# Optimization experiments

Measured on AMD Instinct MI355X. Metric: run time of the kernel, lower is better.

## Reference

```python
import jax, jax.numpy as jnp
import numpy as np

N = 200000      # total nodes
H = 256         # hidden dim
G = 512         # number of graphs (segments)


def setup_inputs() -> dict:
    key = jax.random.key(0)
    ks = jax.random.split(key, 6)
    x = jax.random.normal(ks[0], (N, H), dtype=jnp.float32)
    batch = jnp.sort(jax.random.randint(ks[1], (N,), 0, G, dtype=jnp.int64))
    # attn_gate: Linear(H, H//2) -> Tanh -> Linear(H//2, 1)
    W1 = jax.random.normal(ks[2], (H, H // 2), dtype=jnp.float32) * (1.0 / np.sqrt(H))
    b1 = jnp.zeros((H // 2,), dtype=jnp.float32)
    W2 = jax.random.normal(ks[3], (H // 2, 1), dtype=jnp.float32) * (1.0 / np.sqrt(H // 2))
    b2 = jnp.zeros((1,), dtype=jnp.float32)
    # context_proj: Linear(H, H)
    Wp = jax.random.normal(ks[4], (H, H), dtype=jnp.float32) * (1.0 / np.sqrt(H))
    bp = jnp.zeros((H,), dtype=jnp.float32)
    return {"x": x, "batch": batch, "W1": W1, "b1": b1, "W2": W2, "b2": b2, "Wp": Wp, "bp": bp}


def reference(x, batch, W1, b1, W2, b2, Wp, bp):
    # gating MLP -> per-node scalar score [N, 1]
    s = jnp.tanh(x @ W1 + b1) @ W2 + b2
    # scatter_softmax over segments (numerically stable)
    seg_max = jax.ops.segment_max(s, batch, num_segments=G)        # [G, 1]
    e = jnp.exp(s - seg_max[batch])                                 # [N, 1]
    seg_sum = jax.ops.segment_sum(e, batch, num_segments=G)        # [G, 1]
    w = e / seg_sum[batch]                                          # [N, 1]
    # attention-weighted global add pool -> [G, H]
    graph_emb = jax.ops.segment_sum(x * w, batch, num_segments=G)
    # project and broadcast back to nodes -> [N, H]
    context = graph_emb @ Wp + bp
    return context[batch]
```

## Files before the change

kernel.cpp:

```cpp
#include <hip/hip_runtime.h>
#include <hip/hip_bf16.h>

#define HH 256
#define HJ 128
#define GG 512

typedef __attribute__((ext_vector_type(8))) short short8;
typedef __attribute__((ext_vector_type(4))) float f32x4;

static __device__ __forceinline__ unsigned f2bfu(float f) {
  unsigned u = __builtin_bit_cast(unsigned, f);
  return (u + 0x7FFFu + ((u >> 16) & 1u)) >> 16;
}

static __device__ __forceinline__ uint2 pack4(const float4 f) {
  return make_uint2(f2bfu(f.x) | (f2bfu(f.y) << 16),
                    f2bfu(f.z) | (f2bfu(f.w) << 16));
}

__global__ __launch_bounds__(64) void w1frag_kernel(
    const float* __restrict__ W1, short8* __restrict__ w1a) {
  const int l = threadIdx.x;
  const int kt = blockIdx.x >> 3;
  const int jt = blockIdx.x & 7;
  const int j = jt * 16 + (l & 15);
  const int kb = kt * 32 + (l >> 4) * 8;
  short8 v;
#pragma unroll
  for (int i = 0; i < 8; ++i) v[i] = (short)f2bfu(W1[(size_t)(kb + i) * HJ + j]);
  w1a[blockIdx.x * 64 + l] = v;
}

__global__ __launch_bounds__(256) void segstart_kernel(
    const int* __restrict__ batch, int* __restrict__ segstart, int N, int G) {
  const int n = blockIdx.x * 256 + threadIdx.x;
  if (n >= N) return;
  const int b = batch[n];
  const int p = (n == 0) ? -1 : batch[n - 1];
  for (int g = p + 1; g <= b; ++g) segstart[g] = n;
  if (n == N - 1) {
    for (int g = b + 1; g <= G; ++g) segstart[g] = N;
  }
}

__global__ __launch_bounds__(512) void fused_kernel(
    const float* __restrict__ x, const short8* __restrict__ w1a,
    const float* __restrict__ b1, const float* __restrict__ W2,
    const int* __restrict__ segstart, const float* __restrict__ Wp,
    const float* __restrict__ bp, float4* __restrict__ out4, int N) {
  __shared__ char xb[3 * 32768];
  __shared__ float spart[2][8][64];
  __shared__ float elds[64];
  __shared__ float esums;

  const int tid = threadIdx.x;
  const int l = tid & 63;
  const int w = tid >> 6;
  const int g = blockIdx.x;

  const int n0 = segstart[g];
  const int n1 = segstart[g + 1];
  const int cnt = n1 - n0;
  if (cnt <= 0) return;

  const int ntiles = (cnt + 63) >> 6;
  const float4* x4 = (const float4*)x;

  const int jt0 = w & 3;
  short8 afrag[2][8];
  float4 bb[2], ww[2];
  if (w < 4) {
#pragma unroll
    for (int jj = 0; jj < 2; ++jj) {
      const int jt = jt0 + jj * 4;
#pragma unroll
      for (int kt = 0; kt < 8; ++kt) afrag[jj][kt] = w1a[(kt * 8 + jt) * 64 + l];
      const int j0 = 16 * jt + (l >> 4) * 4;
      bb[jj] = *reinterpret_cast<const float4*>(b1 + j0);
      ww[jj] = *reinterpret_cast<const float4*>(W2 + j0);
    }
  }

  {
    float4 rr[8];
#pragma unroll
    for (int k = 0; k < 8; ++k) {
      const int node = min(n0 + w * 8 + k, N - 1);
      rr[k] = x4[(size_t)node * 64 + l];
    }
#pragma unroll
    for (int k = 0; k < 8; ++k) {
      const int r = w * 8 + k;
      const int swz = (r & 7) << 4;
      *reinterpret_cast<uint2*>(xb + r * 512 + ((l * 8) ^ swz)) = pack4(rr[k]);
    }
  }
  __syncthreads();

  const int c2 = tid & 127;
  const int qh = (tid >> 7) & 1;
  float2 pacc = make_float2(0.f, 0.f);
  float es_acc = 0.f;

  for (int i = 0; i < ntiles; ++i) {
    if (w < 4) {
      const char* xbi = xb + (i % 3) * 32768;
      float* sp = &spart[i & 1][0][0];
#pragma unroll
      for (int nt = 0; nt < 4; ++nt) {
        const int node = nt * 16 + (l & 15);
        const int nb = node * 512;
        const int swz = (node & 7) << 4;
        short8 bfrag[8];
#pragma unroll
        for (int kt = 0; kt < 8; ++kt) {
          bfrag[kt] = *reinterpret_cast<const short8*>(
              xbi + nb + ((kt * 64 + ((l >> 4) << 4)) ^ swz));
        }
#pragma unroll
        for (int jj = 0; jj < 2; ++jj) {
          f32x4 acc = (f32x4)(0.f);
#pragma unroll
          for (int kt = 0; kt < 8; ++kt) {
            acc = __builtin_amdgcn_mfma_f32_16x16x32_bf16(afrag[jj][kt],
                                                          bfrag[kt], acc, 0, 0, 0);
          }
          float t0 = __expf(2.f * (acc[0] + bb[jj].x));
          float t1 = __expf(2.f * (acc[1] + bb[jj].y));
          float t2 = __expf(2.f * (acc[2] + bb[jj].z));
          float t3 = __expf(2.f * (acc[3] + bb[jj].w));
          float ps = (1.f - 2.f / (t0 + 1.f)) * ww[jj].x +
                     (1.f - 2.f / (t1 + 1.f)) * ww[jj].y +
                     (1.f - 2.f / (t2 + 1.f)) * ww[jj].z +
                     (1.f - 2.f / (t3 + 1.f)) * ww[jj].w;
          ps += __shfl_xor(ps, 16, 64);
          ps += __shfl_xor(ps, 32, 64);
          if (l < 16) sp[(jt0 + jj * 4) * 64 + node] = ps;
        }
      }
    } else {
      if (i >= 1) {
        const float* sp = &spart[(i - 1) & 1][0][0];
        float s = 0.f;
#pragma unroll
        for (int jt = 0; jt < 8; ++jt) s += sp[jt * 64 + l];
        const int node = n0 + (i - 1) * 64 + l;
        const float e = (node < n1) ? __expf(s) : 0.f;
        elds[l] = e;
        if (w == 4) es_acc += e;
        const char* xbs = xb + ((i - 1) % 3) * 32768;
#pragma unroll 8
        for (int m = 0; m < 32; ++m) {
          const int n = qh * 32 + m;
          const unsigned v = *reinterpret_cast<const unsigned*>(
              xbs + n * 512 + ((c2 * 4) ^ ((n & 7) << 4)));
          const float ee = elds[n];
          pacc.x = fmaf(__builtin_bit_cast(float, v << 16), ee, pacc.x);
          pacc.y = fmaf(__builtin_bit_cast(float, v & 0xFFFF0000u), ee, pacc.y);
        }
      }
      if (i + 1 < ntiles) {
        char* xbd = xb + ((i + 1) % 3) * 32768;
        const int rb = (w - 4) * 16;
        float4 rr[8];
#pragma unroll
        for (int b = 0; b < 2; ++b) {
#pragma unroll
          for (int k = 0; k < 8; ++k) {
            const int node = min(n0 + (i + 1) * 64 + rb + b * 8 + k, N - 1);
            rr[k] = x4[(size_t)node * 64 + l];
          }
#pragma unroll
          for (int k = 0; k < 8; ++k) {
            const int r = rb + b * 8 + k;
            const int swz = (r & 7) << 4;
            *reinterpret_cast<uint2*>(xbd + r * 512 + ((l * 8) ^ swz)) =
                pack4(rr[k]);
          }
        }
      }
    }
    __syncthreads();
  }

  if (w >= 4) {
    const float* sp = &spart[(ntiles - 1) & 1][0][0];
    float s = 0.f;
#pragma unroll
    for (int jt = 0; jt < 8; ++jt) s += sp[jt * 64 + l];
    const int node = n0 + (ntiles - 1) * 64 + l;
    const float e = (node < n1) ? __expf(s) : 0.f;
    elds[l] = e;
    if (w == 4) es_acc += e;
    const char* xbs = xb + ((ntiles - 1) % 3) * 32768;
#pragma unroll 8
    for (int m = 0; m < 32; ++m) {
      const int n = qh * 32 + m;
      const unsigned v = *reinterpret_cast<const unsigned*>(
          xbs + n * 512 + ((c2 * 4) ^ ((n & 7) << 4)));
      const float ee = elds[n];
      pacc.x = fmaf(__builtin_bit_cast(float, v << 16), ee, pacc.x);
      pacc.y = fmaf(__builtin_bit_cast(float, v & 0xFFFF0000u), ee, pacc.y);
    }
    if (w == 4) {
      float es = es_acc;
      es += __shfl_xor(es, 1, 64);
      es += __shfl_xor(es, 2, 64);
      es += __shfl_xor(es, 4, 64);
      es += __shfl_xor(es, 8, 64);
      es += __shfl_xor(es, 16, 64);
      es += __shfl_xor(es, 32, 64);
      if (l == 0) esums = es;
    }
  }
  __syncthreads();

  float* fbase = (float*)xb;
  if (w >= 4) {
    fbase[qh * 256 + c2 * 2] = pacc.x;
    fbase[qh * 256 + c2 * 2 + 1] = pacc.y;
  }
  __syncthreads();

  float* er = fbase + 512;
  if (tid < HH) {
    const float es = esums;
    const float inv = (es > 0.f) ? 1.f / es : 0.f;
    er[tid] = (fbase[tid] + fbase[256 + tid]) * inv;
  }
  __syncthreads();

  float* pr = fbase + 768;
  {
    const int c = tid & 255;
    const int h2 = tid >> 8;
    float p = 0.f;
    const float* wp = Wp + (size_t)h2 * 128 * HH + c;
#pragma unroll 4
    for (int k = 0; k < 128; ++k) {
      p = fmaf(er[h2 * 128 + k], wp[(size_t)k * HH], p);
    }
    pr[h2 * 256 + c] = p;
  }
  __syncthreads();
  float* ctxl = fbase + 1280;
  if (tid < HH) {
    ctxl[tid] = pr[tid] + pr[256 + tid] + bp[tid];
  }
  __syncthreads();

  {
    const int q = tid & 63;
    const float4 cv = reinterpret_cast<const float4*>(ctxl)[q];
    for (int n = n0 + w; n < n1; n += 8) {
      out4[(size_t)n * 64 + q] = cv;
    }
  }
}

extern "C" void kernel_launch(void* const* d_in, const int* in_sizes, int n_in,
                              void* d_out, int out_size, void* d_ws, size_t ws_size,
                              hipStream_t stream) {
  const float* x = (const float*)d_in[0];
  const int* batch = (const int*)d_in[1];
  const float* W1 = (const float*)d_in[2];
  const float* b1 = (const float*)d_in[3];
  const float* W2 = (const float*)d_in[4];
  const float* Wp = (const float*)d_in[6];
  const float* bp = (const float*)d_in[7];
  float* out = (float*)d_out;

  const int N = in_sizes[1];
  const int G = GG;

  char* wsp = (char*)d_ws;
  short8* w1a = (short8*)wsp;
  size_t off = 4096 * sizeof(short8);
  int* segstart = (int*)(wsp + off);

  w1frag_kernel<<<dim3(64), 64, 0, stream>>>(W1, w1a);
  {
    dim3 grid((N + 255) / 256);
    segstart_kernel<<<grid, 256, 0, stream>>>(batch, segstart, N, G);
  }
  fused_kernel<<<dim3(G), 512, 0, stream>>>(x, w1a, b1, W2, segstart, Wp, bp,
                                            (float4*)out, N);
}
```

Baseline: 116.8 us.

## Double block size to 1024 threads with eight MFMA and eight pooling/loader waves

Each block now launches 1024 threads. Eight waves compute the gating MLP, one 16-column j-tile each, and eight waves handle softmax pooling and the prefetch of the next x tile, so each wave does half its former work. Wave n-tile order is rotated to spread LDS access. The Wp projection is split four ways and the output broadcast uses 16 waves. This shortens each block's serial critical path, but it limits occupancy to one block per CU and adds more sync overhead and register pressure.

```diff
diff --git a/kernel.cpp b/kernel.cpp
--- a/kernel.cpp
+++ b/kernel.cpp
@@ -43,7 +43,7 @@
   }
 }
 
-__global__ __launch_bounds__(512) void fused_kernel(
+__global__ __launch_bounds__(1024, 1) void fused_kernel(
     const float* __restrict__ x, const short8* __restrict__ w1a,
     const float* __restrict__ b1, const float* __restrict__ W2,
     const int* __restrict__ segstart, const float* __restrict__ Wp,
@@ -66,49 +66,46 @@
   const int ntiles = (cnt + 63) >> 6;
   const float4* x4 = (const float4*)x;
 
-  const int jt0 = w & 3;
-  short8 afrag[2][8];
-  float4 bb[2], ww[2];
-  if (w < 4) {
-#pragma unroll
-    for (int jj = 0; jj < 2; ++jj) {
-      const int jt = jt0 + jj * 4;
-#pragma unroll
-      for (int kt = 0; kt < 8; ++kt) afrag[jj][kt] = w1a[(kt * 8 + jt) * 64 + l];
-      const int j0 = 16 * jt + (l >> 4) * 4;
-      bb[jj] = *reinterpret_cast<const float4*>(b1 + j0);
-      ww[jj] = *reinterpret_cast<const float4*>(W2 + j0);
-    }
-  }
-
-  {
-    float4 rr[8];
-#pragma unroll
-    for (int k = 0; k < 8; ++k) {
-      const int node = min(n0 + w * 8 + k, N - 1);
+  short8 afrag[8];
+  float4 bb, ww;
+  if (w < 8) {
+#pragma unroll
+    for (int kt = 0; kt < 8; ++kt) afrag[kt] = w1a[(kt * 8 + w) * 64 + l];
+    const int j0 = 16 * w + (l >> 4) * 4;
+    bb = *reinterpret_cast<const float4*>(b1 + j0);
+    ww = *reinterpret_cast<const float4*>(W2 + j0);
+  }
+
+  {
+    float4 rr[4];
+#pragma unroll
+    for (int k = 0; k < 4; ++k) {
+      const int node = min(n0 + w * 4 + k, N - 1);
       rr[k] = x4[(size_t)node * 64 + l];
     }
 #pragma unroll
-    for (int k = 0; k < 8; ++k) {
-      const int r = w * 8 + k;
+    for (int k = 0; k < 4; ++k) {
+      const int r = w * 4 + k;
       const int swz = (r & 7) << 4;
       *reinterpret_cast<uint2*>(xb + r * 512 + ((l * 8) ^ swz)) = pack4(rr[k]);
     }
   }
   __syncthreads();
 
-  const int c2 = tid & 127;
-  const int qh = (tid >> 7) & 1;
+  const int pid = tid - 512;
+  const int c2 = pid & 127;
+  const int q4 = (pid >> 7) & 3;
   float2 pacc = make_float2(0.f, 0.f);
   float es_acc = 0.f;
 
   for (int i = 0; i < ntiles; ++i) {
-    if (w < 4) {
+    if (w < 8) {
       const char* xbi = xb + (i % 3) * 32768;
       float* sp = &spart[i & 1][0][0];
 #pragma unroll
       for (int nt = 0; nt < 4; ++nt) {
-        const int node = nt * 16 + (l & 15);
+        const int ntw = (nt + w) & 3;
+        const int node = ntw * 16 + (l & 15);
         const int nb = node * 512;
         const int swz = (node & 7) << 4;
         short8 bfrag[8];
@@ -117,26 +114,23 @@
           bfrag[kt] = *reinterpret_cast<const short8*>(
               xbi + nb + ((kt * 64 + ((l >> 4) << 4)) ^ swz));
         }
-#pragma unroll
-        for (int jj = 0; jj < 2; ++jj) {
-          f32x4 acc = (f32x4)(0.f);
-#pragma unroll
-          for (int kt = 0; kt < 8; ++kt) {
-            acc = __builtin_amdgcn_mfma_f32_16x16x32_bf16(afrag[jj][kt],
-                                                          bfrag[kt], acc, 0, 0, 0);
-          }
-          float t0 = __expf(2.f * (acc[0] + bb[jj].x));
-          float t1 = __expf(2.f * (acc[1] + bb[jj].y));
-          float t2 = __expf(2.f * (acc[2] + bb[jj].z));
-          float t3 = __expf(2.f * (acc[3] + bb[jj].w));
-          float ps = (1.f - 2.f / (t0 + 1.f)) * ww[jj].x +
-                     (1.f - 2.f / (t1 + 1.f)) * ww[jj].y +
-                     (1.f - 2.f / (t2 + 1.f)) * ww[jj].z +
-                     (1.f - 2.f / (t3 + 1.f)) * ww[jj].w;
-          ps += __shfl_xor(ps, 16, 64);
-          ps += __shfl_xor(ps, 32, 64);
-          if (l < 16) sp[(jt0 + jj * 4) * 64 + node] = ps;
-        }
+        f32x4 acc = (f32x4)(0.f);
+#pragma unroll
+        for (int kt = 0; kt < 8; ++kt) {
+          acc = __builtin_amdgcn_mfma_f32_16x16x32_bf16(afrag[kt], bfrag[kt],
+                                                        acc, 0, 0, 0);
+        }
+        float t0 = __expf(2.f * (acc[0] + bb.x));
+        float t1 = __expf(2.f * (acc[1] + bb.y));
+        float t2 = __expf(2.f * (acc[2] + bb.z));
+        float t3 = __expf(2.f * (acc[3] + bb.w));
+        float ps = (1.f - 2.f / (t0 + 1.f)) * ww.x +
+                   (1.f - 2.f / (t1 + 1.f)) * ww.y +
+                   (1.f - 2.f / (t2 + 1.f)) * ww.z +
+                   (1.f - 2.f / (t3 + 1.f)) * ww.w;
+        ps += __shfl_xor(ps, 16, 64);
+        ps += __shfl_xor(ps, 32, 64);
+        if (l < 16) sp[w * 64 + node] = ps;
       }
     } else {
       if (i >= 1) {
@@ -147,11 +141,11 @@
         const int node = n0 + (i - 1) * 64 + l;
         const float e = (node < n1) ? __expf(s) : 0.f;
         elds[l] = e;
-        if (w == 4) es_acc += e;
+        if (w == 8) es_acc += e;
         const char* xbs = xb + ((i - 1) % 3) * 32768;
 #pragma unroll 8
-        for (int m = 0; m < 32; ++m) {
-          const int n = qh * 32 + m;
+        for (int m = 0; m < 16; ++m) {
+          const int n = q4 * 16 + m;
           const unsigned v = *reinterpret_cast<const unsigned*>(
               xbs + n * 512 + ((c2 * 4) ^ ((n & 7) << 4)));
           const float ee = elds[n];
@@ -161,29 +155,26 @@
       }
       if (i + 1 < ntiles) {
         char* xbd = xb + ((i + 1) % 3) * 32768;
-        const int rb = (w - 4) * 16;
+        const int rb = (w - 8) * 8;
         float4 rr[8];
 #pragma unroll
-        for (int b = 0; b < 2; ++b) {
-#pragma unroll
-          for (int k = 0; k < 8; ++k) {
-            const int node = min(n0 + (i + 1) * 64 + rb + b * 8 + k, N - 1);
-            rr[k] = x4[(size_t)node * 64 + l];
-          }
-#pragma unroll
-          for (int k = 0; k < 8; ++k) {
-            const int r = rb + b * 8 + k;
-            const int swz = (r & 7) << 4;
-            *reinterpret_cast<uint2*>(xbd + r * 512 + ((l * 8) ^ swz)) =
-                pack4(rr[k]);
-          }
+        for (int k = 0; k < 8; ++k) {
+          const int node = min(n0 + (i + 1) * 64 + rb + k, N - 1);
+          rr[k] = x4[(size_t)node * 64 + l];
+        }
+#pragma unroll
+        for (int k = 0; k < 8; ++k) {
+          const int r = rb + k;
+          const int swz = (r & 7) << 4;
+          *reinterpret_cast<uint2*>(xbd + r * 512 + ((l * 8) ^ swz)) =
+              pack4(rr[k]);
         }
       }
     }
     __syncthreads();
   }
 
-  if (w >= 4) {
+  if (w >= 8) {
     const float* sp = &spart[(ntiles - 1) & 1][0][0];
     float s = 0.f;
 #pragma unroll
@@ -191,18 +182,18 @@
     const int node = n0 + (ntiles - 1) * 64 + l;
     const float e = (node < n1) ? __expf(s) : 0.f;
     elds[l] = e;
-    if (w == 4) es_acc += e;
+    if (w == 8) es_acc += e;
     const char* xbs = xb + ((ntiles - 1) % 3) * 32768;
 #pragma unroll 8
-    for (int m = 0; m < 32; ++m) {
-      const int n = qh * 32 + m;
+    for (int m = 0; m < 16; ++m) {
+      const int n = q4 * 16 + m;
       const unsigned v = *reinterpret_cast<const unsigned*>(
           xbs + n * 512 + ((c2 * 4) ^ ((n & 7) << 4)));
       const float ee = elds[n];
       pacc.x = fmaf(__builtin_bit_cast(float, v << 16), ee, pacc.x);
       pacc.y = fmaf(__builtin_bit_cast(float, v & 0xFFFF0000u), ee, pacc.y);
     }
-    if (w == 4) {
+    if (w == 8) {
       float es = es_acc;
       es += __shfl_xor(es, 1, 64);
       es += __shfl_xor(es, 2, 64);
@@ -216,43 +207,45 @@
   __syncthreads();
 
   float* fbase = (float*)xb;
-  if (w >= 4) {
-    fbase[qh * 256 + c2 * 2] = pacc.x;
-    fbase[qh * 256 + c2 * 2 + 1] = pacc.y;
-  }
-  __syncthreads();
-
-  float* er = fbase + 512;
+  if (w >= 8) {
+    fbase[q4 * 256 + c2 * 2] = pacc.x;
+    fbase[q4 * 256 + c2 * 2 + 1] = pacc.y;
+  }
+  __syncthreads();
+
+  float* er = fbase + 1024;
   if (tid < HH) {
     const float es = esums;
     const float inv = (es > 0.f) ? 1.f / es : 0.f;
-    er[tid] = (fbase[tid] + fbase[256 + tid]) * inv;
-  }
-  __syncthreads();
-
-  float* pr = fbase + 768;
+    er[tid] =
+        (fbase[tid] + fbase[256 + tid] + fbase[512 + tid] + fbase[768 + tid]) *
+        inv;
+  }
+  __syncthreads();
+
+  float* pr = fbase + 1280;
   {
     const int c = tid & 255;
-    const int h2 = tid >> 8;
+    const int h4 = tid >> 8;
     float p = 0.f;
-    const float* wp = Wp + (size_t)h2 * 128 * HH + c;
+    const float* wp = Wp + (size_t)h4 * 64 * HH + c;
 #pragma unroll 4
-    for (int k = 0; k < 128; ++k) {
-      p = fmaf(er[h2 * 128 + k], wp[(size_t)k * HH], p);
-    }
-    pr[h2 * 256 + c] = p;
-  }
-  __syncthreads();
-  float* ctxl = fbase + 1280;
+    for (int k = 0; k < 64; ++k) {
+      p = fmaf(er[h4 * 64 + k], wp[(size_t)k * HH], p);
+    }
+    pr[h4 * 256 + c] = p;
+  }
+  __syncthreads();
+  float* ctxl = fbase + 2304;
   if (tid < HH) {
-    ctxl[tid] = pr[tid] + pr[256 + tid] + bp[tid];
+    ctxl[tid] = pr[tid] + pr[256 + tid] + pr[512 + tid] + pr[768 + tid] + bp[tid];
   }
   __syncthreads();
 
   {
     const int q = tid & 63;
     const float4 cv = reinterpret_cast<const float4*>(ctxl)[q];
-    for (int n = n0 + w; n < n1; n += 8) {
+    for (int n = n0 + w; n < n1; n += 16) {
       out4[(size_t)n * 64 + q] = cv;
     }
   }
@@ -283,6 +276,6 @@
     dim3 grid((N + 255) / 256);
     segstart_kernel<<<grid, 256, 0, stream>>>(batch, segstart, N, G);
   }
-  fused_kernel<<<dim3(G), 512, 0, stream>>>(x, w1a, b1, W2, segstart, Wp, bp,
-                                            (float4*)out, N);
-}
+  fused_kernel<<<dim3(G), 1024, 0, stream>>>(x, w1a, b1, W2, segstart, Wp, bp,
+                                             (float4*)out, N);
+}
```

Result: slower. 146.2 us (+25.2%).
